# Kernel tuning notes

Hardware: AMD Instinct MI355X
Metric: run time of the kernel (lower is better)

Reference implementation:

```python
import jax, jax.numpy as jnp
import numpy as np

BATCH = 8192
N_BANDS = 2000
TARGET = 500
FIRST_HIDDEN = 50
LEAKY_SLOPE = 0.01  # torch LeakyReLU default


def _tridiag_solve(lower, diag, upper, rhs):
    """Thomas algorithm. lower/upper: (n-1,), diag: (n,), rhs: (n, B). Returns (n, B)."""
    dt = rhs.dtype
    up = jnp.concatenate([upper, jnp.zeros((1,), dt)])   # (n,)
    lo = jnp.concatenate([jnp.zeros((1,), dt), lower])   # (n,)

    def fwd(carry, inp):
        cp_prev, dp_prev = carry
        d_i, u_i, l_i, r_i = inp
        m = d_i - l_i * cp_prev
        cp = u_i / m
        dp = (r_i - l_i * dp_prev) / m
        return (cp, dp), (cp, dp)

    init = (jnp.zeros((), dt), jnp.zeros(rhs.shape[1:], dt))
    _, (cps, dps) = jax.lax.scan(fwd, init, (diag, up, lo, rhs))

    def bwd(x_next, inp):
        cp, dp = inp
        x = dp - cp * x_next
        return x, x

    _, xs = jax.lax.scan(bwd, jnp.zeros(rhs.shape[1:], dt), (cps, dps), reverse=True)
    return xs


def natural_cubic_spline_coeffs(times, path):
    """times: (n,), path: (B, n) -> (a, b, two_c, three_d), each (B, n-1)."""
    h = times[1:] - times[:-1]            # (n-1,)
    hr = 1.0 / h
    hr2 = hr * hr
    diffs3 = 3.0 * (path[:, 1:] - path[:, :-1])   # (B, n-1)
    diffs6 = 2.0 * diffs3
    pds = diffs3 * hr2                             # (B, n-1)
    n = path.shape[1]
    diag = (jnp.zeros((n,), path.dtype).at[:-1].set(hr).at[1:].add(hr)) * 2.0
    rhs = jnp.zeros_like(path).at[:, :-1].set(pds).at[:, 1:].add(pds)  # (B, n)
    kd = _tridiag_solve(hr, diag, hr, rhs.T).T     # knot derivatives (B, n)
    a = path[:, :-1]
    b = kd[:, :-1]
    two_c = (diffs6 * hr - 4.0 * kd[:, :-1] - 2.0 * kd[:, 1:]) * hr
    three_d = (-diffs6 * hr + 3.0 * (kd[:, :-1] + kd[:, 1:])) * hr2
    return a, b, two_c, three_d


def spline_evaluate(times, coeffs, t):
    """Evaluate at points t: (T,). Returns (B, T)."""
    a, b, two_c, three_d = coeffs
    idx = jnp.clip(jnp.searchsorted(times, t, side='left') - 1, 0, times.shape[0] - 2)
    frac = t - times[idx]                  # (T,)
    inner = 0.5 * two_c[:, idx] + three_d[:, idx] * frac / 3.0
    inner = b[:, idx] + inner * frac
    return a[:, idx] + inner * frac


def leaky_relu(x):
    return jnp.where(x >= 0, x, LEAKY_SLOPE * x)


def setup_inputs() -> dict:
    key = jax.random.key(0)
    ks = jax.random.split(key, 8)
    return {
        'x': jax.random.uniform(ks[0], (BATCH, N_BANDS), dtype=jnp.float32),
        'raw_index': jax.random.normal(ks[1], (TARGET,), dtype=jnp.float32),
        'W1': jax.random.normal(ks[2], (TARGET, FIRST_HIDDEN), dtype=jnp.float32) * 0.05,
        'b1': jax.random.normal(ks[3], (FIRST_HIDDEN,), dtype=jnp.float32) * 0.05,
        'W2': jax.random.normal(ks[4], (FIRST_HIDDEN, 10), dtype=jnp.float32) * 0.1,
        'b2': jax.random.normal(ks[5], (10,), dtype=jnp.float32) * 0.1,
        'W3': jax.random.normal(ks[6], (10, 1), dtype=jnp.float32) * 0.1,
        'b3': jax.random.normal(ks[7], (1,), dtype=jnp.float32) * 0.1,
    }


def reference(x, raw_index, W1, b1, W2, b2, W3, b3):
    # x: (B, n_bands). Spline is fit along the band axis with knots linspace(0,1,n_bands).
    times = jnp.linspace(0.0, 1.0, x.shape[1]).astype(x.dtype)
    coeffs = natural_cubic_spline_coeffs(times, x)
    # Each BandIndex machine evaluates the spline at sigmoid(raw_index_i) -> batched over all i.
    t_eval = jax.nn.sigmoid(raw_index)             # (T,)
    outputs = spline_evaluate(times, coeffs, t_eval)  # (B, T)
    h = leaky_relu(outputs @ W1 + b1)
    h = leaky_relu(h @ W2 + b2)
    soc_hat = (h @ W3 + b3).reshape(-1)            # (B,)
    return soc_hat
```

## Files before the change

### kernel.cpp

```cpp
#include <hip/hip_runtime.h>

#define NB 2000
#define BATCH 8192
#define NT 500
#define NH1 50
#define NH2 10
#define HRc 1999.0f
#define STEPc (1.0f/1999.0f)
#define LP 520

typedef __attribute__((ext_vector_type(8))) short short8;
typedef __attribute__((ext_vector_type(4))) float f32x4;

__device__ __forceinline__ float b2f(unsigned short u) {
    return __uint_as_float(((unsigned int)u) << 16);
}
__device__ __forceinline__ unsigned short f2b(float f) {
    unsigned int u = __float_as_uint(f);
    return (unsigned short)((u + 0x7FFFu + ((u >> 16) & 1u)) >> 16);
}
__device__ __forceinline__ float ldv(const void* p, int i, int flag) {
    return flag ? b2f(((const unsigned short*)p)[i]) : ((const float*)p)[i];
}
__device__ __forceinline__ int wave_detect(const void* x) {
    const unsigned char* xb = (const unsigned char*)x;
    int lane = threadIdx.x & 63;
    int pred = xb[4 * lane + 1] > 0x3F;
    unsigned long long m = __ballot(pred);
    return (__popcll(m) > 4) ? 0 : 1;
}

__global__ __launch_bounds__(256, 1) void pm_build(
        const void* __restrict__ x, const void* __restrict__ raw_index,
        const void* __restrict__ W1, unsigned int* __restrict__ MB) {
    __shared__ float scS[NT * 35];
    __shared__ int   sbS[512];
    __shared__ float cp_tab[64];
    __shared__ float sc[2];

    int tid = threadIdx.x;
    int flag = wave_detect(x);
    if (tid == 0) {
        double cp = 0.5;
        cp_tab[0] = 0.5f;
        for (int i = 1; i < 64; ++i) { cp = 1.0 / (4.0 - cp); cp_tab[i] = (float)cp; }
        sc[0] = (float)cp;
        sc[1] = (float)(1.0 / (2.0 - cp));
    }
    __syncthreads();
    float c_inf = sc[0], w_last = sc[1];

    #pragma unroll 1
    for (int rep = 0; rep < 2; ++rep) {
        int t = tid + rep * 256;
        if (t < NT) {
            float coef_rel[34];
            #pragma unroll
            for (int k = 0; k < 34; ++k) coef_rel[k] = 0.0f;

            float r = ldv(raw_index, t, flag);
            float v = 1.0f / (1.0f + expf(-r));
            int lo = 0, hi = NB;
            while (lo < hi) {
                int mid = (lo + hi) >> 1;
                float tm = (float)mid * STEPc;
                if (tm < v) lo = mid + 1; else hi = mid;
            }
            int idx = lo - 1;
            idx = idx < 0 ? 0 : (idx > NB - 2 ? NB - 2 : idx);
            float f = v - (float)idx * STEPc;
            float u = f * HRc;
            float A = 1.0f + u * u * (2.0f * u - 3.0f);
            float B = u * u * (3.0f - 2.0f * u);
            float C = f * (1.0f - u) * (1.0f - u);
            float D = f * u * (u - 1.0f);

            const float g3 = 3.0f * HRc * HRc;
            const float invhr = 1.0f / HRc;

            #pragma unroll
            for (int row = 0; row < 2; ++row) {
                int j = idx + row;
                float scale = row ? D : C;
                float z[35];
                #pragma unroll
                for (int q = 0; q < 35; ++q) z[q] = 0.0f;
                float w0 = (j <= NB - 2) ? ((j < 64) ? cp_tab[j] : c_inf) : w_last;
                z[17] = w0 * invhr;
                #pragma unroll
                for (int s = 1; s <= 17; ++s) {
                    int m = j + s;
                    float wm;
                    if (m <= NB - 2)      wm = (m < 64) ? cp_tab[m] : c_inf;
                    else if (m == NB - 1) wm = w_last;
                    else                  wm = 0.0f;
                    z[17 + s] = -wm * z[17 + s - 1];
                }
                #pragma unroll
                for (int s = 16; s >= -17; --s) {
                    int m = j + s;
                    float cpv;
                    if (m >= NB - 1 || m < 0) cpv = 0.0f;
                    else                      cpv = (m < 64) ? cp_tab[m] : c_inf;
                    z[17 + s] = z[17 + s] - cpv * z[17 + s + 1];
                }
                #pragma unroll
                for (int s = -16; s <= 16; ++s) {
                    int m = j + s;
                    float gv = 0.0f;
                    if (m >= 1)      gv += z[17 + s - 1];
                    if (m <= NB - 2) gv -= z[17 + s + 1];
                    if (m == NB - 1) gv += z[17 + s];
                    if (m == 0)      gv -= z[17 + s];
                    gv *= g3;
                    bool valid = (m >= 0) && (m <= NB - 1);
                    coef_rel[s + row + 16] += valid ? scale * gv : 0.0f;
                }
            }
            coef_rel[16] += A;
            coef_rel[17] += B;

            #pragma unroll
            for (int j2 = 0; j2 < 34; ++j2) scS[t * 35 + j2] = coef_rel[j2];
            sbS[t] = idx;
        }
    }
    __syncthreads();

    int k2 = blockIdx.x * 4 + (tid >> 6);
    int h = tid & 63;
    int hh = h < NH1 ? h : NH1 - 1;
    int k0 = 2 * k2;
    float acc0 = 0.0f, acc1 = 0.0f;
    if (k0 < NB) {
        #pragma unroll 4
        for (int t = 0; t < NT; ++t) {
            int idx = sbS[t];
            int rel0 = k0 - idx + 16;
            if (rel0 >= -1 && rel0 < 34) {
                float w1v = ldv(W1, t * NH1 + hh, flag);
                if (rel0 >= 0)  acc0 += scS[t * 35 + rel0] * w1v;
                if (rel0 < 33)  acc1 += scS[t * 35 + rel0 + 1] * w1v;
            }
        }
    }
    bool ok = (h < NH1) && (k0 < NB);
    unsigned int lo16 = ok ? (unsigned int)f2b(acc0) : 0u;
    unsigned int hi16 = ok ? (unsigned int)f2b(acc1) : 0u;
    int kt = k0 >> 5;
    int kr = k0 & 31;
    int gg = kr >> 3;
    int j  = kr & 7;
    int ht = h >> 4;
    int lt = gg * 16 + (h & 15);
    MB[(((kt * 4 + ht) * 64 + lt) << 2) + (j >> 1)] = lo16 | (hi16 << 16);
}

__global__ __launch_bounds__(512, 4) void g_fused(
        const void* __restrict__ x, const unsigned int* __restrict__ MB,
        const void* __restrict__ b1, const void* __restrict__ W2,
        const void* __restrict__ b2, const void* __restrict__ W3,
        const void* __restrict__ b3, void* __restrict__ out) {
    __shared__ __align__(16) unsigned short lx[2][16 * LP];
    __shared__ float red[8][16][68];
    __shared__ float Wmlp[NH1 * NH2 + NH1 + NH2 + NH2 + 1];

    int tid = threadIdx.x;
    int flag = wave_detect(x);

    for (int i = tid; i < NH1 * NH2; i += 512) Wmlp[i] = ldv(W2, i, flag);
    if (tid < NH1) Wmlp[500 + tid] = ldv(b1, tid, flag);
    if (tid < NH2) Wmlp[550 + tid] = ldv(b2, tid, flag);
    if (tid < NH2) Wmlp[560 + tid] = ldv(W3, tid, flag);
    if (tid == 0)  Wmlp[570] = ldv(b3, 0, flag);

    int lane = tid & 63;
    int c16  = tid & 15;
    int g    = (tid >> 4) & 3;
    int w    = tid >> 6;
    int srow = tid >> 5;
    int soff = tid & 31;
    int r0   = blockIdx.x * 16;
    const unsigned short* xs = (const unsigned short*)x;
    const float*          xf = (const float*)x;
    size_t crow = (size_t)(r0 + srow) * NB;

    f32x4 acc[4];
    #pragma unroll
    for (int ht = 0; ht < 4; ++ht) acc[ht] = (f32x4){0.f, 0.f, 0.f, 0.f};

    union AU { uint4 u; short8 s; };
    const uint4* mb4 = (const uint4*)MB;

    if (flag) {
        uint4 pf[8];
        #pragma unroll
        for (int c = 0; c < 4; ++c) {
            int gk0 = c * 512 + soff * 8;
            int gk1 = gk0 + 256;
            pf[2 * c]     = (gk0 + 8 <= NB) ? *(const uint4*)(xs + crow + gk0)
                                            : make_uint4(0u, 0u, 0u, 0u);
            pf[2 * c + 1] = (gk1 + 8 <= NB) ? *(const uint4*)(xs + crow + gk1)
                                            : make_uint4(0u, 0u, 0u, 0u);
        }
        *(uint4*)&lx[0][srow * LP + soff * 8]       = pf[0];
        *(uint4*)&lx[0][srow * LP + soff * 8 + 256] = pf[1];

        int cur = 0;
        #pragma unroll
        for (int c = 0; c < 4; ++c) {
            __syncthreads();
            #pragma unroll
            for (int dk = 0; dk < 2; ++dk) {
                int ktl = 2 * w + dk;
                AU a;
                a.u = *(const uint4*)&lx[cur][c16 * LP + ktl * 32 + g * 8];
                int kt = c * 16 + ktl;
                #pragma unroll
                for (int ht = 0; ht < 4; ++ht) {
                    AU b; b.u = mb4[(kt * 4 + ht) * 64 + lane];
                    acc[ht] = __builtin_amdgcn_mfma_f32_16x16x32_bf16(a.s, b.s, acc[ht], 0, 0, 0);
                }
            }
            if (c < 3) {
                *(uint4*)&lx[cur ^ 1][srow * LP + soff * 8]       = pf[2 * (c + 1)];
                *(uint4*)&lx[cur ^ 1][srow * LP + soff * 8 + 256] = pf[2 * (c + 1) + 1];
            }
            __syncthreads();
            cur ^= 1;
        }
    } else {
        #define LDSEGF(dst, gk) do {                                          \
            int _gk = (gk);                                                   \
            if (_gk + 8 <= NB) {                                              \
                float4 _v0 = *(const float4*)(xf + crow + _gk);               \
                float4 _v1 = *(const float4*)(xf + crow + _gk + 4);           \
                (dst).x = (unsigned)f2b(_v0.x) | ((unsigned)f2b(_v0.y) << 16); \
                (dst).y = (unsigned)f2b(_v0.z) | ((unsigned)f2b(_v0.w) << 16); \
                (dst).z = (unsigned)f2b(_v1.x) | ((unsigned)f2b(_v1.y) << 16); \
                (dst).w = (unsigned)f2b(_v1.z) | ((unsigned)f2b(_v1.w) << 16); \
            } else {                                                          \
                (dst) = make_uint4(0u, 0u, 0u, 0u);                           \
            }                                                                 \
        } while (0)
        {
            uint4 p0, p1;
            LDSEGF(p0, soff * 8);
            LDSEGF(p1, soff * 8 + 256);
            *(uint4*)&lx[0][srow * LP + soff * 8]       = p0;
            *(uint4*)&lx[0][srow * LP + soff * 8 + 256] = p1;
        }
        int cur = 0;
        #pragma unroll
        for (int c = 0; c < 4; ++c) {
            __syncthreads();
            uint4 s0 = make_uint4(0u,0u,0u,0u), s1 = make_uint4(0u,0u,0u,0u);
            if (c < 3) {
                LDSEGF(s0, (c + 1) * 512 + soff * 8);
                LDSEGF(s1, (c + 1) * 512 + soff * 8 + 256);
            }
            #pragma unroll
            for (int dk = 0; dk < 2; ++dk) {
                int ktl = 2 * w + dk;
                AU a;
                a.u = *(const uint4*)&lx[cur][c16 * LP + ktl * 32 + g * 8];
                int kt = c * 16 + ktl;
                #pragma unroll
                for (int ht = 0; ht < 4; ++ht) {
                    AU b; b.u = mb4[(kt * 4 + ht) * 64 + lane];
                    acc[ht] = __builtin_amdgcn_mfma_f32_16x16x32_bf16(a.s, b.s, acc[ht], 0, 0, 0);
                }
            }
            if (c < 3) {
                *(uint4*)&lx[cur ^ 1][srow * LP + soff * 8]       = s0;
                *(uint4*)&lx[cur ^ 1][srow * LP + soff * 8 + 256] = s1;
            }
            __syncthreads();
            cur ^= 1;
        }
        #undef LDSEGF
    }

    #pragma unroll
    for (int ht = 0; ht < 4; ++ht)
        #pragma unroll
        for (int r = 0; r < 4; ++r)
            red[w][g * 4 + r][ht * 16 + c16] = acc[ht][r];
    __syncthreads();

    #pragma unroll
    for (int ii = 0; ii < 2; ++ii) {
        int idx = tid + ii * 512;
        int row = idx >> 6, h = idx & 63;
        float s = 0.0f;
        #pragma unroll
        for (int w2 = 0; w2 < 8; ++w2) s += red[w2][row][h];
        red[0][row][h] = s;
    }
    __syncthreads();

    if (tid < 16) {
        float h1v[NH1];
        #pragma unroll
        for (int h = 0; h < NH1; ++h) {
            float vv = red[0][tid][h] + Wmlp[500 + h];
            h1v[h] = vv >= 0.0f ? vv : 0.01f * vv;
        }
        float o = Wmlp[570];
        for (int j = 0; j < NH2; ++j) {
            float a2 = Wmlp[550 + j];
            #pragma unroll
            for (int h = 0; h < NH1; ++h)
                a2 = fmaf(h1v[h], Wmlp[h * NH2 + j], a2);
            a2 = a2 >= 0.0f ? a2 : 0.01f * a2;
            o = fmaf(a2, Wmlp[560 + j], o);
        }
        int b = r0 + tid;
        if (flag) ((unsigned short*)out)[b] = f2b(o);
        else      ((float*)out)[b] = o;
    }
}

extern "C" void kernel_launch(void* const* d_in, const int* in_sizes, int n_in,
                              void* d_out, int out_size, void* d_ws, size_t ws_size,
                              hipStream_t stream) {
    const void* x   = d_in[0];
    const void* raw = d_in[1];
    const void* W1  = d_in[2];
    const void* b1  = d_in[3];
    const void* W2  = d_in[4];
    const void* b2  = d_in[5];
    const void* W3  = d_in[6];
    const void* b3  = d_in[7];

    float* w = (float*)d_ws;
    unsigned int* MB = (unsigned int*)(w + 17512);

    pm_build<<<256, 256, 0, stream>>>(x, raw, W1, MB);
    g_fused<<<512, 512, 0, stream>>>(x, MB, b1, W2, b2, W3, b3, d_out);
}
```

Baseline: 165.5 us.

## Split stencil build into separate kernel and parallelize M build across waves

The fused pm_build kernel made every one of its 256 blocks recompute all 500 spline stencil rows, then reduce over all 500 targets in a single wave per output column. That work is now split in two. A small kernel computes each stencil once into workspace. A second kernel gives each column pair its own block and splits the target loop across four waves, combining them with a shared-memory reduction. This removes the redundant per-block recomputation and adds parallelism, at the cost of an extra launch and a global-memory round trip for the coefficients.

```diff
diff --git a/kernel.cpp b/kernel.cpp
--- a/kernel.cpp
+++ b/kernel.cpp
@@ -30,16 +30,13 @@
     return (__popcll(m) > 4) ? 0 : 1;
 }
 
-__global__ __launch_bounds__(256, 1) void pm_build(
-        const void* __restrict__ x, const void* __restrict__ raw_index,
-        const void* __restrict__ W1, unsigned int* __restrict__ MB) {
-    __shared__ float scS[NT * 35];
-    __shared__ int   sbS[512];
+__global__ __launch_bounds__(64, 1) void p1_stencil(
+        const void* __restrict__ xdet, const void* __restrict__ raw_index,
+        float* __restrict__ S_coef, int* __restrict__ S_base) {
     __shared__ float cp_tab[64];
     __shared__ float sc[2];
-
     int tid = threadIdx.x;
-    int flag = wave_detect(x);
+    int flag = wave_detect(xdet);
     if (tid == 0) {
         double cp = 0.5;
         cp_tab[0] = 0.5f;
@@ -48,112 +45,129 @@
         sc[1] = (float)(1.0 / (2.0 - cp));
     }
     __syncthreads();
+    int t = blockIdx.x * 64 + tid;
+    if (t >= NT) return;
     float c_inf = sc[0], w_last = sc[1];
 
-    #pragma unroll 1
-    for (int rep = 0; rep < 2; ++rep) {
-        int t = tid + rep * 256;
-        if (t < NT) {
-            float coef_rel[34];
-            #pragma unroll
-            for (int k = 0; k < 34; ++k) coef_rel[k] = 0.0f;
-
-            float r = ldv(raw_index, t, flag);
-            float v = 1.0f / (1.0f + expf(-r));
-            int lo = 0, hi = NB;
-            while (lo < hi) {
-                int mid = (lo + hi) >> 1;
-                float tm = (float)mid * STEPc;
-                if (tm < v) lo = mid + 1; else hi = mid;
-            }
-            int idx = lo - 1;
-            idx = idx < 0 ? 0 : (idx > NB - 2 ? NB - 2 : idx);
-            float f = v - (float)idx * STEPc;
-            float u = f * HRc;
-            float A = 1.0f + u * u * (2.0f * u - 3.0f);
-            float B = u * u * (3.0f - 2.0f * u);
-            float C = f * (1.0f - u) * (1.0f - u);
-            float D = f * u * (u - 1.0f);
-
-            const float g3 = 3.0f * HRc * HRc;
-            const float invhr = 1.0f / HRc;
-
-            #pragma unroll
-            for (int row = 0; row < 2; ++row) {
-                int j = idx + row;
-                float scale = row ? D : C;
-                float z[35];
-                #pragma unroll
-                for (int q = 0; q < 35; ++q) z[q] = 0.0f;
-                float w0 = (j <= NB - 2) ? ((j < 64) ? cp_tab[j] : c_inf) : w_last;
-                z[17] = w0 * invhr;
-                #pragma unroll
-                for (int s = 1; s <= 17; ++s) {
-                    int m = j + s;
-                    float wm;
-                    if (m <= NB - 2)      wm = (m < 64) ? cp_tab[m] : c_inf;
-                    else if (m == NB - 1) wm = w_last;
-                    else                  wm = 0.0f;
-                    z[17 + s] = -wm * z[17 + s - 1];
-                }
-                #pragma unroll
-                for (int s = 16; s >= -17; --s) {
-                    int m = j + s;
-                    float cpv;
-                    if (m >= NB - 1 || m < 0) cpv = 0.0f;
-                    else                      cpv = (m < 64) ? cp_tab[m] : c_inf;
-                    z[17 + s] = z[17 + s] - cpv * z[17 + s + 1];
-                }
-                #pragma unroll
-                for (int s = -16; s <= 16; ++s) {
-                    int m = j + s;
-                    float gv = 0.0f;
-                    if (m >= 1)      gv += z[17 + s - 1];
-                    if (m <= NB - 2) gv -= z[17 + s + 1];
-                    if (m == NB - 1) gv += z[17 + s];
-                    if (m == 0)      gv -= z[17 + s];
-                    gv *= g3;
-                    bool valid = (m >= 0) && (m <= NB - 1);
-                    coef_rel[s + row + 16] += valid ? scale * gv : 0.0f;
-                }
-            }
-            coef_rel[16] += A;
-            coef_rel[17] += B;
-
-            #pragma unroll
-            for (int j2 = 0; j2 < 34; ++j2) scS[t * 35 + j2] = coef_rel[j2];
-            sbS[t] = idx;
-        }
-    }
-    __syncthreads();
-
-    int k2 = blockIdx.x * 4 + (tid >> 6);
+    float coef_rel[34];
+    #pragma unroll
+    for (int k = 0; k < 34; ++k) coef_rel[k] = 0.0f;
+
+    float r = ldv(raw_index, t, flag);
+    float v = 1.0f / (1.0f + expf(-r));
+    int lo = 0, hi = NB;
+    while (lo < hi) {
+        int mid = (lo + hi) >> 1;
+        float tm = (float)mid * STEPc;
+        if (tm < v) lo = mid + 1; else hi = mid;
+    }
+    int idx = lo - 1;
+    idx = idx < 0 ? 0 : (idx > NB - 2 ? NB - 2 : idx);
+    float f = v - (float)idx * STEPc;
+    float u = f * HRc;
+    float A = 1.0f + u * u * (2.0f * u - 3.0f);
+    float B = u * u * (3.0f - 2.0f * u);
+    float C = f * (1.0f - u) * (1.0f - u);
+    float D = f * u * (u - 1.0f);
+
+    const float g3 = 3.0f * HRc * HRc;
+    const float invhr = 1.0f / HRc;
+
+    #pragma unroll
+    for (int row = 0; row < 2; ++row) {
+        int j = idx + row;
+        float scale = row ? D : C;
+        float z[35];
+        #pragma unroll
+        for (int q = 0; q < 35; ++q) z[q] = 0.0f;
+        float w0 = (j <= NB - 2) ? ((j < 64) ? cp_tab[j] : c_inf) : w_last;
+        z[17] = w0 * invhr;
+        #pragma unroll
+        for (int s = 1; s <= 17; ++s) {
+            int m = j + s;
+            float wm;
+            if (m <= NB - 2)      wm = (m < 64) ? cp_tab[m] : c_inf;
+            else if (m == NB - 1) wm = w_last;
+            else                  wm = 0.0f;
+            z[17 + s] = -wm * z[17 + s - 1];
+        }
+        #pragma unroll
+        for (int s = 16; s >= -17; --s) {
+            int m = j + s;
+            float cpv;
+            if (m >= NB - 1 || m < 0) cpv = 0.0f;
+            else                      cpv = (m < 64) ? cp_tab[m] : c_inf;
+            z[17 + s] = z[17 + s] - cpv * z[17 + s + 1];
+        }
+        #pragma unroll
+        for (int s = -16; s <= 16; ++s) {
+            int m = j + s;
+            float gv = 0.0f;
+            if (m >= 1)      gv += z[17 + s - 1];
+            if (m <= NB - 2) gv -= z[17 + s + 1];
+            if (m == NB - 1) gv += z[17 + s];
+            if (m == 0)      gv -= z[17 + s];
+            gv *= g3;
+            bool valid = (m >= 0) && (m <= NB - 1);
+            coef_rel[s + row + 16] += valid ? scale * gv : 0.0f;
+        }
+    }
+    coef_rel[16] += A;
+    coef_rel[17] += B;
+
+    #pragma unroll
+    for (int j = 0; j < 34; ++j) S_coef[t * 34 + j] = coef_rel[j];
+    S_base[t] = idx;
+}
+
+__global__ __launch_bounds__(256) void m_build2(
+        const void* __restrict__ xdet, const void* __restrict__ W1,
+        const float* __restrict__ S_coef, const int* __restrict__ S_base,
+        unsigned int* __restrict__ MB) {
+    __shared__ int sb[NT];
+    __shared__ float red0[4][64];
+    __shared__ float red1[4][64];
+    int tid = threadIdx.x;
+    int flag = wave_detect(xdet);
+    for (int i = tid; i < NT; i += 256) sb[i] = S_base[i];
+    __syncthreads();
+    int wv = tid >> 6;
     int h = tid & 63;
     int hh = h < NH1 ? h : NH1 - 1;
+    int k2 = blockIdx.x;
     int k0 = 2 * k2;
     float acc0 = 0.0f, acc1 = 0.0f;
     if (k0 < NB) {
+        int t0 = wv * 125, t1 = t0 + 125;
         #pragma unroll 4
-        for (int t = 0; t < NT; ++t) {
-            int idx = sbS[t];
+        for (int t = t0; t < t1; ++t) {
+            int idx = sb[t];
             int rel0 = k0 - idx + 16;
             if (rel0 >= -1 && rel0 < 34) {
                 float w1v = ldv(W1, t * NH1 + hh, flag);
-                if (rel0 >= 0)  acc0 += scS[t * 35 + rel0] * w1v;
-                if (rel0 < 33)  acc1 += scS[t * 35 + rel0 + 1] * w1v;
-            }
-        }
-    }
-    bool ok = (h < NH1) && (k0 < NB);
-    unsigned int lo16 = ok ? (unsigned int)f2b(acc0) : 0u;
-    unsigned int hi16 = ok ? (unsigned int)f2b(acc1) : 0u;
-    int kt = k0 >> 5;
-    int kr = k0 & 31;
-    int gg = kr >> 3;
-    int j  = kr & 7;
-    int ht = h >> 4;
-    int lt = gg * 16 + (h & 15);
-    MB[(((kt * 4 + ht) * 64 + lt) << 2) + (j >> 1)] = lo16 | (hi16 << 16);
+                if (rel0 >= 0)  acc0 += S_coef[t * 34 + rel0] * w1v;
+                if (rel0 < 33)  acc1 += S_coef[t * 34 + rel0 + 1] * w1v;
+            }
+        }
+    }
+    red0[wv][h] = acc0;
+    red1[wv][h] = acc1;
+    __syncthreads();
+    if (tid < 64) {
+        float a0 = ((red0[0][tid] + red0[1][tid]) + red0[2][tid]) + red0[3][tid];
+        float a1 = ((red1[0][tid] + red1[1][tid]) + red1[2][tid]) + red1[3][tid];
+        int hh2 = tid;
+        bool ok = (hh2 < NH1) && (k0 < NB);
+        unsigned int lo16 = ok ? (unsigned int)f2b(a0) : 0u;
+        unsigned int hi16 = ok ? (unsigned int)f2b(a1) : 0u;
+        int kt = k0 >> 5;
+        int kr = k0 & 31;
+        int gg = kr >> 3;
+        int j  = kr & 7;
+        int ht = hh2 >> 4;
+        int lt = gg * 16 + (hh2 & 15);
+        MB[(((kt * 4 + ht) * 64 + lt) << 2) + (j >> 1)] = lo16 | (hi16 << 16);
+    }
 }
 
 __global__ __launch_bounds__(512, 4) void g_fused(
@@ -333,9 +347,12 @@
     const void* W3  = d_in[6];
     const void* b3  = d_in[7];
 
-    float* w = (float*)d_ws;
+    float* w      = (float*)d_ws;
+    int*   S_base = (int*)w;
+    float* S_coef = w + 512;
     unsigned int* MB = (unsigned int*)(w + 17512);
 
-    pm_build<<<256, 256, 0, stream>>>(x, raw, W1, MB);
+    p1_stencil<<<8, 64, 0, stream>>>(x, raw, S_coef, S_base);
+    m_build2<<<1024, 256, 0, stream>>>(x, W1, S_coef, S_base, MB);
     g_fused<<<512, 512, 0, stream>>>(x, MB, b1, W2, b2, W3, b3, d_out);
 }
```

Measured after the change: 136.9 us (median of 2 runs). 1.21x faster.
